# Kernel optimization log

Hardware: AMD Instinct MI355X
Metric: run time of the kernel (lower is better)

The kernel has to match this reference:

```python
import jax, jax.numpy as jnp
import numpy as np

TAU = 1.0
NUM_CENTROIDS = 8
COMMITMENT_COST = 0.25


def setup_inputs() -> dict:
    key = jax.random.key(0)
    kx, kc = jax.random.split(key)
    B, T, D = 8, 2048, 512
    K = 4096  # codebook_size
    x = jax.random.normal(kx, (B, T, D), dtype=jnp.float32)
    # variance_scaling(1.0, fan_in, uniform): limit = sqrt(3/D)
    limit = np.sqrt(3.0 / D).astype(np.float32)
    codebook = jax.random.uniform(kc, (K, D), dtype=jnp.float32, minval=-limit, maxval=limit)
    return {"x": x, "codebook": codebook}


def _squared_euclidean_distance(a, b):
    # a: [N, D], b: [K, D] -> [N, K]
    a2 = jnp.sum(a * a, axis=-1, keepdims=True)          # [N, 1]
    b2 = jnp.sum(b * b, axis=-1)                          # [K]
    ab = a @ b.T                                          # [N, K]
    return a2 - 2.0 * ab + b2


def reference(x, codebook):
    B, T, D = x.shape
    K = codebook.shape[0]
    flat = x.reshape(-1, D)
    distances = _squared_euclidean_distance(flat, codebook).reshape(B, T, K)
    weights = jax.nn.softmax(-distances / TAU, axis=-1)
    top_weights, top_indices = jax.lax.top_k(weights, NUM_CENTROIDS)  # [B,T,k]
    top_weights = top_weights / jnp.sum(top_weights, axis=-1, keepdims=True)
    # decode_ids: weighted sum of gathered codebook rows (== one-hot einsum)
    gathered = jnp.take(codebook, top_indices, axis=0)                # [B,T,k,D]
    quantized = jnp.einsum('btk,btkd->btd', top_weights, gathered)
    # train=True losses (entropy_loss_ratio == 0 -> skipped)
    e_latent_loss = jnp.mean((jax.lax.stop_gradient(quantized) - x) ** 2) * COMMITMENT_COST
    q_latent_loss = jnp.mean((quantized - jax.lax.stop_gradient(x)) ** 2)
    loss = e_latent_loss.astype(jnp.float32) + q_latent_loss.astype(jnp.float32)
    # straight-through estimator
    quantized = x + jax.lax.stop_gradient(quantized - x)
    return quantized, loss
```

## Files before the change

### kernel.cpp

```cpp
#include <hip/hip_runtime.h>
#include <stdint.h>

#define D_DIM 512
#define K_CB  4096
#define N_TOK 16384
#define TOPK  8

#define TOKB  32
#define NPASS 16
#define NSEL  16

typedef __attribute__((ext_vector_type(4)))  int    i32x4;
typedef __attribute__((ext_vector_type(8)))  int    i32x8;
typedef __attribute__((ext_vector_type(16))) float  f32x16;
typedef __attribute__((ext_vector_type(4)))  float  f32x4;

template<int N>
__device__ __forceinline__ void inskey(unsigned int k, unsigned int (&ts)[N]) {
    #pragma unroll
    for (int q = 0; q < N; ++q) {
        unsigned int hi = ts[q] > k ? ts[q] : k;
        unsigned int lo = ts[q] > k ? k : ts[q];
        ts[q] = hi; k = lo;
    }
}

__device__ __forceinline__ f32x16 mfma_step(i32x4 al, i32x4 ah, i32x4 bl, i32x4 bh,
                                            f32x16 acc) {
    return __builtin_amdgcn_mfma_scale_f32_32x32x64_f8f6f4(
        __builtin_shufflevector(al, ah, 0,1,2,3,4,5,6,7),
        __builtin_shufflevector(bl, bh, 0,1,2,3,4,5,6,7),
        acc, 0, 0, 0, 0x7F7F7F7F, 0, 0x7F7F7F7F);
}

__global__ __launch_bounds__(256) void conv_cb_kernel(
    const float* __restrict__ cb, unsigned char* __restrict__ cbf8,
    float* __restrict__ cnorm, float* __restrict__ loss,
    unsigned int* __restrict__ ticket) {
    const int t = threadIdx.x, gb = blockIdx.x;
    if (gb == 0 && t == 0) { *loss = 0.f; *ticket = 0u; }
    const int r16 = t >> 4, c = t & 15;
    const int row = gb * 16 + r16;
    const float* src = cb + (size_t)row * D_DIM + c * 32;
    float sq = 0.f;
    unsigned int d[8];
    #pragma unroll
    for (int i = 0; i < 8; ++i) {
        float4 v = ((const float4*)src)[i];
        sq += v.x*v.x + v.y*v.y + v.z*v.z + v.w*v.w;
        int dd = __builtin_amdgcn_cvt_pk_fp8_f32(64.f * v.x, 64.f * v.y, 0, false);
        dd     = __builtin_amdgcn_cvt_pk_fp8_f32(64.f * v.z, 64.f * v.w, dd, true);
        d[i] = (unsigned int)dd;
    }
    sq += __shfl_down(sq, 8, 16);
    sq += __shfl_down(sq, 4, 16);
    sq += __shfl_down(sq, 2, 16);
    sq += __shfl_down(sq, 1, 16);
    if (c == 0) cnorm[row] = sq;
    const int g = row >> 5, row32 = row & 31;
    const int s = c >> 1, khalf = c & 1;
    unsigned char* base = cbf8 + (size_t)g * 16384 + (size_t)s * 2048
                        + (size_t)(khalf * 32 + row32) * 16;
    i32x4 lo = {(int)d[0], (int)d[1], (int)d[2], (int)d[3]};
    i32x4 hi = {(int)d[4], (int)d[5], (int)d[6], (int)d[7]};
    *(i32x4*)(base)        = lo;
    *(i32x4*)(base + 1024) = hi;
}

__global__ __launch_bounds__(512, 4) void vq_fused(
    const float* __restrict__ x, const float* __restrict__ cb,
    const unsigned char* __restrict__ cbf8, const float* __restrict__ cnorm,
    float* __restrict__ out, float* __restrict__ loss_acc,
    unsigned int* __restrict__ ticket)
{
    __shared__ union {
        unsigned char xs8[TOKB * D_DIM];
        unsigned int  keys[256 * 32];
    } u;
    __shared__ float ncn[K_CB];
    __shared__ unsigned int pk[TOKB * 65];
    __shared__ int   tki[TOKB * 17];
    __shared__ float tks[TOKB * 17];
    __shared__ float tkw[TOKB * TOPK];
    __shared__ int   tkif[TOKB * TOPK];
    __shared__ float redbuf[8];

    const int t    = threadIdx.x;
    const int lane = t & 63;
    const int w    = t >> 6;
    const int m32  = lane & 31;
    const int half = lane >> 5;
    const int tok0 = blockIdx.x * TOKB;

    const char* cb8l = (const char*)cbf8 + (size_t)lane * 16;

    {
        const int token = t >> 4, c = t & 15;
        const int s2 = c >> 1, lh = c & 1;
        const f32x4* src = (const f32x4*)(x + (size_t)(tok0 + token) * D_DIM + c * 32);
        unsigned int d[8];
        #pragma unroll
        for (int i = 0; i < 8; ++i) {
            f32x4 v = src[i];
            int dd = __builtin_amdgcn_cvt_pk_fp8_f32(16.f * v.x, 16.f * v.y, 0, false);
            dd     = __builtin_amdgcn_cvt_pk_fp8_f32(16.f * v.z, 16.f * v.w, dd, true);
            d[i] = (unsigned int)dd;
        }
        unsigned char* base = u.xs8 + s2 * 2048 + (lh * 32 + token) * 16;
        i32x4 lo = {(int)d[0], (int)d[1], (int)d[2], (int)d[3]};
        i32x4 hi = {(int)d[4], (int)d[5], (int)d[6], (int)d[7]};
        *(i32x4*)(base)        = lo;
        *(i32x4*)(base + 1024) = hi;
    }
    {
        float4 v0 = ((const float4*)cnorm)[t];
        float4 v1 = ((const float4*)cnorm)[t + 512];
        float4 n0 = {32768.f - 512.f * v0.x, 32768.f - 512.f * v0.y,
                     32768.f - 512.f * v0.z, 32768.f - 512.f * v0.w};
        float4 n1 = {32768.f - 512.f * v1.x, 32768.f - 512.f * v1.y,
                     32768.f - 512.f * v1.z, 32768.f - 512.f * v1.w};
        *(float4*)&ncn[t * 4]         = n0;
        *(float4*)&ncn[(t + 512) * 4] = n1;
    }
    __syncthreads();

    i32x4 breg[8][2];
    {
        const unsigned char* pb = u.xs8 + lane * 16;
        #pragma unroll
        for (int s = 0; s < 8; ++s) {
            breg[s][0] = *(const i32x4*)(pb + s * 2048);
            breg[s][1] = *(const i32x4*)(pb + s * 2048 + 1024);
        }
    }

    unsigned int tsA[8], tsB[8];
    #pragma unroll
    for (int i = 0; i < 8; ++i) { tsA[i] = 0u; tsB[i] = 0u; }

    for (int pp = 0; pp < NPASS; ++pp) {
        const int p  = (pp + 2 * w) & 15;
        const int ga = p * 8 + w;
        f32x16 acc;
        #pragma unroll
        for (int g = 0; g < 4; ++g) {
            float4 n0 = *(const float4*)&ncn[ga * 32 + g * 8 + 4 * half];
            acc[g*4+0]=n0.x; acc[g*4+1]=n0.y; acc[g*4+2]=n0.z; acc[g*4+3]=n0.w;
        }
        const char* ab = cb8l + (size_t)ga * 16384;
        __builtin_amdgcn_s_setprio(1);
        #pragma unroll
        for (int s = 0; s < 8; ++s) {
            i32x4 al = *(const i32x4*)(ab + s * 2048);
            i32x4 ah = *(const i32x4*)(ab + s * 2048 + 1024);
            acc = mfma_step(al, ah, breg[s][0], breg[s][1], acc);
        }
        __builtin_amdgcn_s_setprio(0);
        const unsigned int K0 = 4095u - (unsigned int)(ga * 32) - 4u * (unsigned int)half;
        if ((pp & 1) == 0) {
            #pragma unroll
            for (int r = 0; r < 16; ++r) {
                const unsigned int cr = (unsigned int)((r & 3) + 8 * (r >> 2));
                inskey((__float_as_uint(acc[r]) & 0xFFFFF000u) | (K0 - cr), tsA);
            }
        } else {
            #pragma unroll
            for (int r = 0; r < 16; ++r) {
                const unsigned int cr = (unsigned int)((r & 3) + 8 * (r >> 2));
                inskey((__float_as_uint(acc[r]) & 0xFFFFF000u) | (K0 - cr), tsB);
            }
        }
    }

    __syncthreads();
    {
        const int L0 = w * 4 + half * 2;
        #pragma unroll
        for (int e = 0; e < 8; ++e) {
            u.keys[(L0 * 8 + e) * 32 + m32]       = tsA[e];
            u.keys[((L0 + 1) * 8 + e) * 32 + m32] = tsB[e];
        }
    }
    __syncthreads();
    if (t < 128) {
        const int token = t >> 2, sub = t & 3;
        unsigned int bs[16];
        #pragma unroll
        for (int i = 0; i < 16; ++i) bs[i] = 0u;
        #pragma unroll 2
        for (int k = 0; k < 64; ++k) inskey(u.keys[(sub * 64 + k) * 32 + token], bs);
        #pragma unroll
        for (int e = 0; e < 16; ++e) pk[token * 65 + sub * 16 + e] = bs[e];
    }
    __syncthreads();
    if (t < TOKB) {
        unsigned int bs[NSEL];
        #pragma unroll
        for (int i = 0; i < NSEL; ++i) bs[i] = 0u;
        #pragma unroll 2
        for (int k = 0; k < 64; ++k) inskey(pk[t * 65 + k], bs);
        #pragma unroll
        for (int r = 0; r < NSEL; ++r) tki[t * 17 + r] = 4095 - (int)(bs[r] & 0xFFFu);
    }
    __syncthreads();
    {
        const int token = t >> 4, sl = t & 15;
        const f32x4* xr = (const f32x4*)(x + (size_t)(tok0 + token) * D_DIM);
        f32x4 xv[8];
        #pragma unroll
        for (int i = 0; i < 8; ++i) xv[i] = xr[sl + 16 * i];
        #pragma unroll
        for (int hh = 0; hh < 2; ++hh) {
            float pd[8];
            #pragma unroll
            for (int e = 0; e < 8; ++e) {
                const int idx = tki[token * 17 + hh * 8 + e];
                const f32x4* cr = (const f32x4*)(cb + (size_t)idx * D_DIM);
                float dot = 0.f;
                #pragma unroll
                for (int i = 0; i < 8; ++i) {
                    f32x4 cv = cr[sl + 16 * i];
                    dot += xv[i].x*cv.x + xv[i].y*cv.y + xv[i].z*cv.z + xv[i].w*cv.w;
                }
                pd[e] = dot;
            }
            #pragma unroll
            for (int e = 0; e < 8; ++e) {
                pd[e] += __shfl_down(pd[e], 8, 16);
                pd[e] += __shfl_down(pd[e], 4, 16);
                pd[e] += __shfl_down(pd[e], 2, 16);
                pd[e] += __shfl_down(pd[e], 1, 16);
            }
            if (sl == 0) {
                #pragma unroll
                for (int e = 0; e < 8; ++e)
                    tks[token * 17 + hh * 8 + e] =
                        2.f * pd[e] - cnorm[tki[token * 17 + hh * 8 + e]];
            }
        }
    }
    __syncthreads();
    if (t < TOKB) {
        unsigned int bs[8];
        #pragma unroll
        for (int i = 0; i < 8; ++i) bs[i] = 0u;
        #pragma unroll
        for (int e = 0; e < NSEL; ++e) {
            unsigned int uu = __float_as_uint(tks[t * 17 + e]);
            uu ^= (unsigned int)((int)uu >> 31) | 0x80000000u;
            inskey((uu & 0xFFFFFFF0u) | (unsigned int)e, bs);
        }
        const float m = tks[t * 17 + (int)(bs[0] & 15u)];
        float wv[TOPK], sum = 0.f;
        int ids[TOPK];
        #pragma unroll
        for (int r = 0; r < TOPK; ++r) {
            const int e = (int)(bs[r] & 15u);
            wv[r] = __expf(tks[t * 17 + e] - m); sum += wv[r];
            ids[r] = tki[t * 17 + e];
        }
        const float inv = 1.f / sum;
        #pragma unroll
        for (int r = 0; r < TOPK; ++r) {
            tkw[t * TOPK + r] = wv[r] * inv;
            tkif[t * TOPK + r] = ids[r];
        }
    }
    __syncthreads();
    float lsum = 0.f;
    #pragma unroll 1
    for (int it = 0; it < (TOKB * (D_DIM / 4)) / 512; ++it) {
        const int p = it * 512 + t;
        const int token = p >> 7, d4 = p & 127;
        float4 q = {0.f, 0.f, 0.f, 0.f};
        #pragma unroll
        for (int e = 0; e < TOPK; ++e) {
            const float wv = tkw[token * TOPK + e];
            const int  idx = tkif[token * TOPK + e];
            const float4 cv = ((const float4*)cb)[(size_t)idx * (D_DIM / 4) + d4];
            q.x += wv * cv.x; q.y += wv * cv.y; q.z += wv * cv.z; q.w += wv * cv.w;
        }
        const size_t go = (size_t)(tok0 + token) * (D_DIM / 4) + d4;
        f32x4 xv = __builtin_nontemporal_load((const f32x4*)x + go);
        const float ex = q.x - xv.x, ey = q.y - xv.y, ez = q.z - xv.z, ew = q.w - xv.w;
        lsum += ex*ex + ey*ey + ez*ez + ew*ew;
        f32x4 qv = {q.x, q.y, q.z, q.w};
        __builtin_nontemporal_store(qv, (f32x4*)out + go);
    }
    #pragma unroll
    for (int off = 32; off > 0; off >>= 1) lsum += __shfl_down(lsum, off, 64);
    if (lane == 0) redbuf[w] = lsum;
    __syncthreads();
    if (t == 0) {
        float s = 0.f;
        #pragma unroll
        for (int i = 0; i < 8; ++i) s += redbuf[i];
        atomicAdd(loss_acc, s);
        __threadfence();
        unsigned int prev = atomicAdd(ticket, 1u);
        if (prev == (unsigned int)(gridDim.x - 1)) {
            __threadfence();
            float total = atomicAdd(loss_acc, 0.f);
            out[(size_t)N_TOK * D_DIM] = 1.25f * total / (float)((size_t)N_TOK * D_DIM);
        }
    }
}

extern "C" void kernel_launch(void* const* d_in, const int* in_sizes, int n_in,
                              void* d_out, int out_size, void* d_ws, size_t ws_size,
                              hipStream_t stream) {
    const float* x  = (const float*)d_in[0];
    const float* cb = (const float*)d_in[1];
    float* out = (float*)d_out;

    char* ws = (char*)d_ws;
    unsigned char* cbf8   = (unsigned char*)ws;
    float*         cnorm  = (float*)(ws + 2097152);
    float*         loss   = (float*)(ws + 2113536);
    unsigned int*  ticket = (unsigned int*)(ws + 2113600);

    conv_cb_kernel<<<256, 256, 0, stream>>>(cb, cbf8, cnorm, loss, ticket);
    vq_fused<<<N_TOK / TOKB, 512, 0, stream>>>(x, cb, cbf8, cnorm, out, loss, ticket);
}
```

Baseline: 237.7 us.

## Split fused VQ kernel into candidate-selection and fp32 rescoring epilogue kernels

Splits the single fused kernel into two launches. The first runs the fp8 distance scan and the candidate top-16 selection, then writes the indices to a global workspace. The second reloads those indices, rescores them in fp32, does the softmax over the top-8, the weighted gather and the loss reduction. The aim is to shrink the LDS footprint and register pressure of the main kernel and improve its occupancy. The cost is an extra launch plus a round trip through global memory for the candidate indices.

```diff
diff --git a/kernel.cpp b/kernel.cpp
--- a/kernel.cpp
+++ b/kernel.cpp
@@ -67,11 +67,9 @@
     *(i32x4*)(base + 1024) = hi;
 }
 
-__global__ __launch_bounds__(512, 4) void vq_fused(
-    const float* __restrict__ x, const float* __restrict__ cb,
-    const unsigned char* __restrict__ cbf8, const float* __restrict__ cnorm,
-    float* __restrict__ out, float* __restrict__ loss_acc,
-    unsigned int* __restrict__ ticket)
+__global__ __launch_bounds__(512, 4) void vq_main(
+    const float* __restrict__ x, const unsigned char* __restrict__ cbf8,
+    const float* __restrict__ cnorm, int* __restrict__ tki_g)
 {
     __shared__ union {
         unsigned char xs8[TOKB * D_DIM];
@@ -79,11 +77,6 @@
     } u;
     __shared__ float ncn[K_CB];
     __shared__ unsigned int pk[TOKB * 65];
-    __shared__ int   tki[TOKB * 17];
-    __shared__ float tks[TOKB * 17];
-    __shared__ float tkw[TOKB * TOPK];
-    __shared__ int   tkif[TOKB * TOPK];
-    __shared__ float redbuf[8];
 
     const int t    = threadIdx.x;
     const int lane = t & 63;
@@ -200,9 +193,32 @@
         #pragma unroll 2
         for (int k = 0; k < 64; ++k) inskey(pk[t * 65 + k], bs);
         #pragma unroll
-        for (int r = 0; r < NSEL; ++r) tki[t * 17 + r] = 4095 - (int)(bs[r] & 0xFFFu);
-    }
-    __syncthreads();
+        for (int r = 0; r < NSEL; ++r)
+            tki_g[(size_t)blockIdx.x * (TOKB * NSEL) + t * NSEL + r] =
+                4095 - (int)(bs[r] & 0xFFFu);
+    }
+}
+
+__global__ __launch_bounds__(512) void vq_epi(
+    const float* __restrict__ x, const float* __restrict__ cb,
+    const float* __restrict__ cnorm, const int* __restrict__ tki_g,
+    float* __restrict__ out, float* __restrict__ loss_acc,
+    unsigned int* __restrict__ ticket)
+{
+    __shared__ int   tkl[TOKB * NSEL];
+    __shared__ float tks[TOKB * 17];
+    __shared__ float tkw[TOKB * TOPK];
+    __shared__ int   tkif[TOKB * TOPK];
+    __shared__ float redbuf[8];
+
+    const int t    = threadIdx.x;
+    const int lane = t & 63;
+    const int w    = t >> 6;
+    const int tok0 = blockIdx.x * TOKB;
+
+    tkl[t] = tki_g[(size_t)blockIdx.x * (TOKB * NSEL) + t];
+    __syncthreads();
+
     {
         const int token = t >> 4, sl = t & 15;
         const f32x4* xr = (const f32x4*)(x + (size_t)(tok0 + token) * D_DIM);
@@ -214,7 +230,7 @@
             float pd[8];
             #pragma unroll
             for (int e = 0; e < 8; ++e) {
-                const int idx = tki[token * 17 + hh * 8 + e];
+                const int idx = tkl[token * NSEL + hh * 8 + e];
                 const f32x4* cr = (const f32x4*)(cb + (size_t)idx * D_DIM);
                 float dot = 0.f;
                 #pragma unroll
@@ -235,7 +251,7 @@
                 #pragma unroll
                 for (int e = 0; e < 8; ++e)
                     tks[token * 17 + hh * 8 + e] =
-                        2.f * pd[e] - cnorm[tki[token * 17 + hh * 8 + e]];
+                        2.f * pd[e] - cnorm[tkl[token * NSEL + hh * 8 + e]];
             }
         }
     }
@@ -257,7 +273,7 @@
         for (int r = 0; r < TOPK; ++r) {
             const int e = (int)(bs[r] & 15u);
             wv[r] = __expf(tks[t * 17 + e] - m); sum += wv[r];
-            ids[r] = tki[t * 17 + e];
+            ids[r] = tkl[t * NSEL + e];
         }
         const float inv = 1.f / sum;
         #pragma unroll
@@ -318,7 +334,9 @@
     float*         cnorm  = (float*)(ws + 2097152);
     float*         loss   = (float*)(ws + 2113536);
     unsigned int*  ticket = (unsigned int*)(ws + 2113600);
+    int*           tki_g  = (int*)(ws + 2113664);
 
     conv_cb_kernel<<<256, 256, 0, stream>>>(cb, cbf8, cnorm, loss, ticket);
-    vq_fused<<<N_TOK / TOKB, 512, 0, stream>>>(x, cb, cbf8, cnorm, out, loss, ticket);
-}
+    vq_main<<<N_TOK / TOKB, 512, 0, stream>>>(x, cbf8, cnorm, tki_g);
+    vq_epi<<<N_TOK / TOKB, 512, 0, stream>>>(x, cb, cnorm, tki_g, out, loss, ticket);
+}
```

Result: no change. 240.3 us (+1.1%).
